# Performance work log

Hardware: AMD Instinct MI355X
Metric: run time of the kernel (lower is better)

Reference implementation:

```python
import jax, jax.numpy as jnp
import numpy as np

T = 10
CH, H, W = 16, 16, 264  # torch grid_sample sees view(1,16,16,264) as N,C,H,W
L, C = 256, 264


def _warp(img, pose):
    """Replicates F.affine_grid + F.grid_sample (bilinear, zeros padding,
    align_corners=False) on img of shape (CH,H,W) with pose=(dx,dy,dyaw)."""
    dx, dy, yaw = pose[0], pose[1], pose[2]
    cos, sin = jnp.cos(yaw), jnp.sin(yaw)
    # normalized base grid, align_corners=False: (2i+1)/N - 1
    xs = (2.0 * jnp.arange(W, dtype=img.dtype) + 1.0) / W - 1.0  # (W,)
    ys = (2.0 * jnp.arange(H, dtype=img.dtype) + 1.0) / H - 1.0  # (H,)
    gx = cos * xs[None, :] + sin * ys[:, None] + dx   # (H,W)
    gy = -sin * xs[None, :] + cos * ys[:, None] + dy  # (H,W)
    # unnormalize (align_corners=False)
    ix = ((gx + 1.0) * W - 1.0) * 0.5
    iy = ((gy + 1.0) * H - 1.0) * 0.5
    ix0 = jnp.floor(ix); iy0 = jnp.floor(iy)
    ix1 = ix0 + 1.0;     iy1 = iy0 + 1.0
    wx1 = ix - ix0; wx0 = 1.0 - wx1
    wy1 = iy - iy0; wy0 = 1.0 - wy1

    def gather(xf, yf):
        inb = (xf >= 0) & (xf < W) & (yf >= 0) & (yf < H)
        xi = jnp.clip(xf.astype(jnp.int32), 0, W - 1)
        yi = jnp.clip(yf.astype(jnp.int32), 0, H - 1)
        v = img[:, yi, xi]                      # (CH,H,W)
        return v * inb.astype(img.dtype)        # zero padding

    out = (gather(ix0, iy0) * (wx0 * wy0)
           + gather(ix1, iy0) * (wx1 * wy0)
           + gather(ix0, iy1) * (wx0 * wy1)
           + gather(ix1, iy1) * (wx1 * wy1))
    return out  # (CH,H,W)


def _forward(fuse_feature, delta_ego_pos):
    ff = fuse_feature                              # (10,256,264)
    dp = delta_ego_pos                             # (10,3)
    ff_sp = ff.reshape(T, CH, H, W)
    # prefix sums: P[k] = sum(dp[0:k]); cumulative pose for (b,t) = -sum(dp[t-1:b])
    P = jnp.concatenate([jnp.zeros((1, 3), dp.dtype), jnp.cumsum(dp, axis=0)], axis=0)
    bs = jnp.repeat(jnp.arange(T), T - 1)          # (90,) frame index
    ts = jnp.tile(jnp.arange(1, T), T)             # (90,) past-frame offset t in [1,9]
    poses = -(P[bs] - P[ts - 1])                   # (90,3)
    valid = (ts <= bs)                             # n_valid_past(b) = b
    src = ff_sp[ts]                                # (90,CH,H,W)
    warped = jax.vmap(_warp)(src, poses)           # (90,CH,H,W)
    warped = warped * valid[:, None, None, None].astype(ff.dtype)
    aligned = jnp.zeros((T, T, CH, H, W), ff.dtype)
    aligned = aligned.at[bs, (T - 1) - ts].set(warped)
    aligned = aligned.at[:, T - 1].set(ff_sp)      # current frame, unwarped
    # (B,T,L*C) self-attention fusion
    tb = aligned.reshape(T, T, L * C)
    scores = jnp.einsum('btd,bsd->bts', tb, tb)
    attn = jax.nn.softmax(scores, axis=-1)
    fused = jnp.einsum('bts,bsd->btd', attn, tb)
    fused = fused.mean(axis=1)                     # (B, L*C)
    return fused.reshape(T, L, C)                  # (10,256,264)


def setup_inputs() -> dict:
    key = jax.random.key(0)
    k1, k2 = jax.random.split(key)
    # scale features so the d=67584 dot products don't saturate the softmax
    fuse_feature = jax.random.normal(k1, (T, L, C), dtype=jnp.float32) * 0.02
    delta_ego_pos = jax.random.normal(k2, (T, 3), dtype=jnp.float32) * 0.1
    return {"fuse_feature": fuse_feature, "delta_ego_pos": delta_ego_pos}


def reference(fuse_feature, delta_ego_pos):
    return _forward(fuse_feature, delta_ego_pos)
```

## Files before the change

kernel.cpp:

```cpp
#include <hip/hip_runtime.h>
#include <math.h>

#define TT 10
#define CHN 16
#define HH 16
#define WW 264
#define HW (HH*WW)
#define DD (CHN*HW)
#define NPAIR 90
#define NCHUNK 33
#define CHUNK (DD/NCHUNK)
#define NACC 55

__global__ void meta_kernel(const float* __restrict__ dp, float4* __restrict__ meta) {
    int i = threadIdx.x;
    if (i >= NPAIR) return;
    int b  = i / 9;
    int ts = i % 9 + 1;
    float ax = 0.f, ay = 0.f, az = 0.f;
    for (int j = 0; j < ts - 1; ++j) { ax += dp[j*3]; ay += dp[j*3+1]; az += dp[j*3+2]; }
    float bx = 0.f, by = 0.f, bz = 0.f;
    for (int j = 0; j < b; ++j)      { bx += dp[j*3]; by += dp[j*3+1]; bz += dp[j*3+2]; }
    float dx  = ax - bx;
    float dy  = ay - by;
    float yaw = az - bz;
    float c = (float)cos((double)yaw);
    float s = (float)sin((double)yaw);
    meta[i] = make_float4(dx, dy, c, s);
}

__global__ __launch_bounds__(256) void build_tb_kernel(const float* __restrict__ ff,
                                                       const float4* __restrict__ meta,
                                                       float* __restrict__ tb) {
    int p = blockIdx.x * 256 + threadIdx.x;
    if (p >= HW) return;
    int s = blockIdx.y, b = blockIdx.z;
    float* dst = tb + (size_t)(b*TT + s)*DD + p;

    if (s == TT - 1) {
        const float* src = ff + (size_t)b*DD + p;
        #pragma unroll
        for (int ch = 0; ch < CHN; ++ch) dst[ch*HW] = src[ch*HW];
        return;
    }
    int ts = (TT - 1) - s;
    if (ts > b) {
        #pragma unroll
        for (int ch = 0; ch < CHN; ++ch) dst[ch*HW] = 0.f;
        return;
    }
    float4 m = meta[b*9 + (ts - 1)];
    int y = p / WW, x = p - y*WW;
    float xs = (2.f*(float)x + 1.f)/(float)WW - 1.f;
    float ys = (2.f*(float)y + 1.f)/(float)HH - 1.f;
    float gx =  m.z*xs + m.w*ys + m.x;
    float gy = -m.w*xs + m.z*ys + m.y;
    float ix = ((gx + 1.f)*(float)WW - 1.f)*0.5f;
    float iy = ((gy + 1.f)*(float)HH - 1.f)*0.5f;
    float ix0 = floorf(ix), iy0 = floorf(iy);
    float ix1 = ix0 + 1.f,  iy1 = iy0 + 1.f;
    float wx1 = ix - ix0, wx0 = 1.f - wx1;
    float wy1 = iy - iy0, wy0 = 1.f - wy1;

    bool inx0 = (ix0 >= 0.f) && (ix0 < (float)WW);
    bool inx1 = (ix1 >= 0.f) && (ix1 < (float)WW);
    bool iny0 = (iy0 >= 0.f) && (iy0 < (float)HH);
    bool iny1 = (iy1 >= 0.f) && (iy1 < (float)HH);
    int xi0 = min(max((int)ix0, 0), WW - 1);
    int xi1 = min(max((int)ix1, 0), WW - 1);
    int yi0 = min(max((int)iy0, 0), HH - 1);
    int yi1 = min(max((int)iy1, 0), HH - 1);

    float w00 = (inx0 && iny0) ? wx0*wy0 : 0.f;
    float w10 = (inx1 && iny0) ? wx1*wy0 : 0.f;
    float w01 = (inx0 && iny1) ? wx0*wy1 : 0.f;
    float w11 = (inx1 && iny1) ? wx1*wy1 : 0.f;
    int o00 = yi0*WW + xi0, o10 = yi0*WW + xi1;
    int o01 = yi1*WW + xi0, o11 = yi1*WW + xi1;

    const float* src = ff + (size_t)ts*DD;
    #pragma unroll
    for (int ch = 0; ch < CHN; ++ch) {
        const float* sc = src + ch*HW;
        float v = sc[o00]*w00 + sc[o10]*w10 + sc[o01]*w01 + sc[o11]*w11;
        dst[ch*HW] = v;
    }
}

__global__ __launch_bounds__(256) void gram_kernel(const float* __restrict__ tb,
                                                   float* __restrict__ partial) {
    int chunk = blockIdx.x, b = blockIdx.y;
    int tid = threadIdx.x;
    const float* base = tb + (size_t)b*TT*DD + chunk*CHUNK;

    float acc[NACC];
    #pragma unroll
    for (int k = 0; k < NACC; ++k) acc[k] = 0.f;

    for (int it = 0; it < CHUNK/256; ++it) {
        int d = it*256 + tid;
        float v[TT];
        #pragma unroll
        for (int t = 0; t < TT; ++t) v[t] = base[(size_t)t*DD + d];
        int k = 0;
        #pragma unroll
        for (int t = 0; t < TT; ++t)
            #pragma unroll
            for (int s2 = t; s2 < TT; ++s2)
                acc[k++] += v[t]*v[s2];
    }

    __shared__ float red[NACC*4];
    int lane = tid & 63, wv = tid >> 6;
    #pragma unroll
    for (int k = 0; k < NACC; ++k) {
        float a = acc[k];
        #pragma unroll
        for (int off = 32; off > 0; off >>= 1) a += __shfl_down(a, off);
        if (lane == 0) red[k*4 + wv] = a;
    }
    __syncthreads();
    if (tid < NACC) {
        float a = red[tid*4] + red[tid*4+1] + red[tid*4+2] + red[tid*4+3];
        partial[((size_t)b*NCHUNK + chunk)*NACC + tid] = a;
    }
}

__global__ void weights_kernel(const float* __restrict__ partial, float* __restrict__ w) {
    __shared__ float ws[TT*TT];
    int tid = threadIdx.x;
    if (tid < TT*TT) ws[tid] = 0.f;
    __syncthreads();
    if (tid < TT*TT) {
        int b = tid / TT, t = tid % TT;
        float sc[TT];
        for (int s = 0; s < TT; ++s) {
            int a0 = min(t, s), a1 = max(t, s);
            int k = a0*TT - a0*(a0 - 1)/2 + (a1 - a0);
            float sum = 0.f;
            for (int c = 0; c < NCHUNK; ++c)
                sum += partial[((size_t)b*NCHUNK + c)*NACC + k];
            sc[s] = sum;
        }
        float mx = sc[0];
        for (int s = 1; s < TT; ++s) mx = fmaxf(mx, sc[s]);
        float e[TT]; float den = 0.f;
        for (int s = 0; s < TT; ++s) { e[s] = expf(sc[s] - mx); den += e[s]; }
        float inv = 1.f / den;
        for (int s = 0; s < TT; ++s) atomicAdd(&ws[b*TT + s], e[s]*inv*0.1f);
    }
    __syncthreads();
    if (tid < TT*TT) w[tid] = ws[tid];
}

__global__ __launch_bounds__(256) void out_kernel(const float* __restrict__ tb,
                                                  const float* __restrict__ w,
                                                  float* __restrict__ out) {
    int b = blockIdx.y;
    int d = blockIdx.x*256 + threadIdx.x;
    __shared__ float wl[TT];
    if (threadIdx.x < TT) wl[threadIdx.x] = w[b*TT + threadIdx.x];
    __syncthreads();
    const float* base = tb + (size_t)b*TT*DD + d;
    float acc = 0.f;
    #pragma unroll
    for (int s = 0; s < TT; ++s) acc += wl[s]*base[(size_t)s*DD];
    out[(size_t)b*DD + d] = acc;
}

extern "C" void kernel_launch(void* const* d_in, const int* in_sizes, int n_in,
                              void* d_out, int out_size, void* d_ws, size_t ws_size,
                              hipStream_t stream) {
    const float* ff = (const float*)d_in[0];
    const float* dp = (const float*)d_in[1];
    float* out = (float*)d_out;

    char* ws = (char*)d_ws;
    float4* meta   = (float4*)ws;
    float* tb      = (float*)(ws + 4096);
    float* partial = (float*)(ws + 4096 + (size_t)TT*TT*DD*sizeof(float));
    float* w       = (float*)(ws + 4096 + (size_t)TT*TT*DD*sizeof(float) + 81920);

    meta_kernel   <<<1, 128, 0, stream>>>(dp, meta);
    build_tb_kernel<<<dim3((HW + 255)/256, TT, TT), 256, 0, stream>>>(ff, meta, tb);
    gram_kernel   <<<dim3(NCHUNK, TT), 256, 0, stream>>>(tb, partial);
    weights_kernel<<<1, 128, 0, stream>>>(partial, w);
    out_kernel    <<<dim3(DD/256, TT), 256, 0, stream>>>(tb, w, out);
}
```

Before: 104.3 us.

## Fuse warp into gram and output kernels, drop materialized aligned tensor

Removes the 27 MB aligned tensor and the separate meta and build kernels. The gram and output kernels now compute the bilinear warp offsets and weights per pixel on the fly and gather straight from the input features. In the output kernel the softmax weights are folded into the bilinear weights. The warp work is recomputed twice in exchange, and per-thread register pressure rises from the 10x4 offset and weight arrays.

After: 109.9 us. +5.4%, slower.

```diff
diff --git a/kernel.cpp b/kernel.cpp
--- a/kernel.cpp
+++ b/kernel.cpp
@@ -7,101 +7,85 @@
 #define WW 264
 #define HW (HH*WW)
 #define DD (CHN*HW)
-#define NPAIR 90
-#define NCHUNK 33
-#define CHUNK (DD/NCHUNK)
+#define NBLK ((HW+255)/256)
 #define NACC 55
 
-__global__ void meta_kernel(const float* __restrict__ dp, float4* __restrict__ meta) {
-    int i = threadIdx.x;
-    if (i >= NPAIR) return;
-    int b  = i / 9;
-    int ts = i % 9 + 1;
-    float ax = 0.f, ay = 0.f, az = 0.f;
-    for (int j = 0; j < ts - 1; ++j) { ax += dp[j*3]; ay += dp[j*3+1]; az += dp[j*3+2]; }
-    float bx = 0.f, by = 0.f, bz = 0.f;
-    for (int j = 0; j < b; ++j)      { bx += dp[j*3]; by += dp[j*3+1]; bz += dp[j*3+2]; }
-    float dx  = ax - bx;
-    float dy  = ay - by;
-    float yaw = az - bz;
-    float c = (float)cos((double)yaw);
-    float s = (float)sin((double)yaw);
-    meta[i] = make_float4(dx, dy, c, s);
-}
-
-__global__ __launch_bounds__(256) void build_tb_kernel(const float* __restrict__ ff,
-                                                       const float4* __restrict__ meta,
-                                                       float* __restrict__ tb) {
-    int p = blockIdx.x * 256 + threadIdx.x;
-    if (p >= HW) return;
-    int s = blockIdx.y, b = blockIdx.z;
-    float* dst = tb + (size_t)(b*TT + s)*DD + p;
-
-    if (s == TT - 1) {
-        const float* src = ff + (size_t)b*DD + p;
+__device__ __forceinline__ void slot_setup(int b, int p, bool act,
+                                           const float4* __restrict__ pose,
+                                           int off[TT][4], float wgt[TT][4]) {
+    int y = p / WW, x = p - y*WW;
+    #pragma unroll
+    for (int s = 0; s < TT; ++s) {
         #pragma unroll
-        for (int ch = 0; ch < CHN; ++ch) dst[ch*HW] = src[ch*HW];
-        return;
-    }
-    int ts = (TT - 1) - s;
-    if (ts > b) {
-        #pragma unroll
-        for (int ch = 0; ch < CHN; ++ch) dst[ch*HW] = 0.f;
-        return;
-    }
-    float4 m = meta[b*9 + (ts - 1)];
-    int y = p / WW, x = p - y*WW;
-    float xs = (2.f*(float)x + 1.f)/(float)WW - 1.f;
-    float ys = (2.f*(float)y + 1.f)/(float)HH - 1.f;
-    float gx =  m.z*xs + m.w*ys + m.x;
-    float gy = -m.w*xs + m.z*ys + m.y;
-    float ix = ((gx + 1.f)*(float)WW - 1.f)*0.5f;
-    float iy = ((gy + 1.f)*(float)HH - 1.f)*0.5f;
-    float ix0 = floorf(ix), iy0 = floorf(iy);
-    float ix1 = ix0 + 1.f,  iy1 = iy0 + 1.f;
-    float wx1 = ix - ix0, wx0 = 1.f - wx1;
-    float wy1 = iy - iy0, wy0 = 1.f - wy1;
-
-    bool inx0 = (ix0 >= 0.f) && (ix0 < (float)WW);
-    bool inx1 = (ix1 >= 0.f) && (ix1 < (float)WW);
-    bool iny0 = (iy0 >= 0.f) && (iy0 < (float)HH);
-    bool iny1 = (iy1 >= 0.f) && (iy1 < (float)HH);
-    int xi0 = min(max((int)ix0, 0), WW - 1);
-    int xi1 = min(max((int)ix1, 0), WW - 1);
-    int yi0 = min(max((int)iy0, 0), HH - 1);
-    int yi1 = min(max((int)iy1, 0), HH - 1);
-
-    float w00 = (inx0 && iny0) ? wx0*wy0 : 0.f;
-    float w10 = (inx1 && iny0) ? wx1*wy0 : 0.f;
-    float w01 = (inx0 && iny1) ? wx0*wy1 : 0.f;
-    float w11 = (inx1 && iny1) ? wx1*wy1 : 0.f;
-    int o00 = yi0*WW + xi0, o10 = yi0*WW + xi1;
-    int o01 = yi1*WW + xi0, o11 = yi1*WW + xi1;
-
-    const float* src = ff + (size_t)ts*DD;
-    #pragma unroll
-    for (int ch = 0; ch < CHN; ++ch) {
-        const float* sc = src + ch*HW;
-        float v = sc[o00]*w00 + sc[o10]*w10 + sc[o01]*w01 + sc[o11]*w11;
-        dst[ch*HW] = v;
+        for (int j = 0; j < 4; ++j) { off[s][j] = 0; wgt[s][j] = 0.f; }
+        if (!act) continue;
+        if (s == TT-1) { off[s][0] = b*DD + p; wgt[s][0] = 1.f; continue; }
+        int ts = (TT-1) - s;
+        if (ts > b) continue;
+        float4 m = pose[ts-1];
+        float xs = (2.f*(float)x + 1.f)/(float)WW - 1.f;
+        float ys = (2.f*(float)y + 1.f)/(float)HH - 1.f;
+        float gx =  m.z*xs + m.w*ys + m.x;
+        float gy = -m.w*xs + m.z*ys + m.y;
+        float ix = ((gx + 1.f)*(float)WW - 1.f)*0.5f;
+        float iy = ((gy + 1.f)*(float)HH - 1.f)*0.5f;
+        float ix0f = floorf(ix), iy0f = floorf(iy);
+        float wx1 = ix - ix0f, wx0 = 1.f - wx1;
+        float wy1 = iy - iy0f, wy0 = 1.f - wy1;
+        int ix0 = (int)ix0f, iy0 = (int)iy0f;
+        int ix1 = ix0 + 1,   iy1 = iy0 + 1;
+        bool inx0 = (ix0 >= 0) && (ix0 < WW);
+        bool inx1 = (ix1 >= 0) && (ix1 < WW);
+        bool iny0 = (iy0 >= 0) && (iy0 < HH);
+        bool iny1 = (iy1 >= 0) && (iy1 < HH);
+        int xi0 = min(max(ix0, 0), WW-1), xi1 = min(max(ix1, 0), WW-1);
+        int yi0 = min(max(iy0, 0), HH-1), yi1 = min(max(iy1, 0), HH-1);
+        int base = ts*DD;
+        off[s][0] = base + yi0*WW + xi0; wgt[s][0] = (inx0 && iny0) ? wx0*wy0 : 0.f;
+        off[s][1] = base + yi0*WW + xi1; wgt[s][1] = (inx1 && iny0) ? wx1*wy0 : 0.f;
+        off[s][2] = base + yi1*WW + xi0; wgt[s][2] = (inx0 && iny1) ? wx0*wy1 : 0.f;
+        off[s][3] = base + yi1*WW + xi1; wgt[s][3] = (inx1 && iny1) ? wx1*wy1 : 0.f;
     }
 }
 
-__global__ __launch_bounds__(256) void gram_kernel(const float* __restrict__ tb,
-                                                   float* __restrict__ partial) {
-    int chunk = blockIdx.x, b = blockIdx.y;
-    int tid = threadIdx.x;
-    const float* base = tb + (size_t)b*TT*DD + chunk*CHUNK;
+__device__ __forceinline__ void pose_setup(const float* __restrict__ dp, int b,
+                                           float4* __restrict__ pose) {
+    if (threadIdx.x < TT-1) {
+        int ts = (int)threadIdx.x + 1;
+        float ax = 0.f, ay = 0.f, az = 0.f;
+        for (int j = 0; j < ts-1; ++j) { ax += dp[3*j]; ay += dp[3*j+1]; az += dp[3*j+2]; }
+        float bx = 0.f, by = 0.f, bz = 0.f;
+        for (int j = 0; j < b; ++j)    { bx += dp[3*j]; by += dp[3*j+1]; bz += dp[3*j+2]; }
+        float yaw = az - bz;
+        pose[threadIdx.x] = make_float4(ax - bx, ay - by,
+                                        (float)cos((double)yaw), (float)sin((double)yaw));
+    }
+}
+
+__global__ __launch_bounds__(256) void gram_fused_kernel(const float* __restrict__ ff,
+                                                         const float* __restrict__ dp,
+                                                         float* __restrict__ partial) {
+    int b = blockIdx.y;
+    int p = blockIdx.x*256 + threadIdx.x;
+    __shared__ float4 pose[TT-1];
+    pose_setup(dp, b, pose);
+    __syncthreads();
+
+    bool act = p < HW;
+    int off[TT][4]; float wgt[TT][4];
+    slot_setup(b, p, act, pose, off, wgt);
 
     float acc[NACC];
     #pragma unroll
     for (int k = 0; k < NACC; ++k) acc[k] = 0.f;
 
-    for (int it = 0; it < CHUNK/256; ++it) {
-        int d = it*256 + tid;
+    for (int ch = 0; ch < CHN; ++ch) {
+        const float* fc = ff + ch*HW;
         float v[TT];
         #pragma unroll
-        for (int t = 0; t < TT; ++t) v[t] = base[(size_t)t*DD + d];
+        for (int s = 0; s < TT; ++s)
+            v[s] = fc[off[s][0]]*wgt[s][0] + fc[off[s][1]]*wgt[s][1]
+                 + fc[off[s][2]]*wgt[s][2] + fc[off[s][3]]*wgt[s][3];
         int k = 0;
         #pragma unroll
         for (int t = 0; t < TT; ++t)
@@ -111,18 +95,19 @@
     }
 
     __shared__ float red[NACC*4];
-    int lane = tid & 63, wv = tid >> 6;
+    int lane = threadIdx.x & 63, wv = threadIdx.x >> 6;
     #pragma unroll
     for (int k = 0; k < NACC; ++k) {
         float a = acc[k];
         #pragma unroll
-        for (int off = 32; off > 0; off >>= 1) a += __shfl_down(a, off);
+        for (int o = 32; o > 0; o >>= 1) a += __shfl_down(a, o);
         if (lane == 0) red[k*4 + wv] = a;
     }
     __syncthreads();
-    if (tid < NACC) {
-        float a = red[tid*4] + red[tid*4+1] + red[tid*4+2] + red[tid*4+3];
-        partial[((size_t)b*NCHUNK + chunk)*NACC + tid] = a;
+    if (threadIdx.x < NACC) {
+        float a = red[threadIdx.x*4] + red[threadIdx.x*4+1]
+                + red[threadIdx.x*4+2] + red[threadIdx.x*4+3];
+        partial[((size_t)b*NBLK + blockIdx.x)*NACC + threadIdx.x] = a;
     }
 }
 
@@ -138,8 +123,8 @@
             int a0 = min(t, s), a1 = max(t, s);
             int k = a0*TT - a0*(a0 - 1)/2 + (a1 - a0);
             float sum = 0.f;
-            for (int c = 0; c < NCHUNK; ++c)
-                sum += partial[((size_t)b*NCHUNK + c)*NACC + k];
+            for (int c = 0; c < NBLK; ++c)
+                sum += partial[((size_t)b*NBLK + c)*NACC + k];
             sc[s] = sum;
         }
         float mx = sc[0];
@@ -153,19 +138,38 @@
     if (tid < TT*TT) w[tid] = ws[tid];
 }
 
-__global__ __launch_bounds__(256) void out_kernel(const float* __restrict__ tb,
-                                                  const float* __restrict__ w,
-                                                  float* __restrict__ out) {
+__global__ __launch_bounds__(256) void out_fused_kernel(const float* __restrict__ ff,
+                                                        const float* __restrict__ dp,
+                                                        const float* __restrict__ w,
+                                                        float* __restrict__ out) {
     int b = blockIdx.y;
-    int d = blockIdx.x*256 + threadIdx.x;
+    int p = blockIdx.x*256 + threadIdx.x;
+    __shared__ float4 pose[TT-1];
     __shared__ float wl[TT];
+    pose_setup(dp, b, pose);
     if (threadIdx.x < TT) wl[threadIdx.x] = w[b*TT + threadIdx.x];
     __syncthreads();
-    const float* base = tb + (size_t)b*TT*DD + d;
-    float acc = 0.f;
+
+    bool act = p < HW;
+    int off[TT][4]; float wgt[TT][4];
+    slot_setup(b, p, act, pose, off, wgt);
     #pragma unroll
-    for (int s = 0; s < TT; ++s) acc += wl[s]*base[(size_t)s*DD];
-    out[(size_t)b*DD + d] = acc;
+    for (int s = 0; s < TT; ++s) {
+        float wb = wl[s];
+        #pragma unroll
+        for (int j = 0; j < 4; ++j) wgt[s][j] *= wb;
+    }
+
+    if (!act) return;
+    for (int ch = 0; ch < CHN; ++ch) {
+        const float* fc = ff + ch*HW;
+        float o = 0.f;
+        #pragma unroll
+        for (int s = 0; s < TT; ++s)
+            o += fc[off[s][0]]*wgt[s][0] + fc[off[s][1]]*wgt[s][1]
+               + fc[off[s][2]]*wgt[s][2] + fc[off[s][3]]*wgt[s][3];
+        out[(size_t)b*DD + ch*HW + p] = o;
+    }
 }
 
 extern "C" void kernel_launch(void* const* d_in, const int* in_sizes, int n_in,
@@ -176,14 +180,10 @@
     float* out = (float*)d_out;
 
     char* ws = (char*)d_ws;
-    float4* meta   = (float4*)ws;
-    float* tb      = (float*)(ws + 4096);
-    float* partial = (float*)(ws + 4096 + (size_t)TT*TT*DD*sizeof(float));
-    float* w       = (float*)(ws + 4096 + (size_t)TT*TT*DD*sizeof(float) + 81920);
+    float* partial = (float*)ws;
+    float* w       = (float*)(ws + 65536);
 
-    meta_kernel   <<<1, 128, 0, stream>>>(dp, meta);
-    build_tb_kernel<<<dim3((HW + 255)/256, TT, TT), 256, 0, stream>>>(ff, meta, tb);
-    gram_kernel   <<<dim3(NCHUNK, TT), 256, 0, stream>>>(tb, partial);
-    weights_kernel<<<1, 128, 0, stream>>>(partial, w);
-    out_kernel    <<<dim3(DD/256, TT), 256, 0, stream>>>(tb, w, out);
+    gram_fused_kernel<<<dim3(NBLK, TT), 256, 0, stream>>>(ff, dp, partial);
+    weights_kernel   <<<1, 128, 0, stream>>>(partial, w);
+    out_fused_kernel <<<dim3(NBLK, TT), 256, 0, stream>>>(ff, dp, w, out);
 }
```
